# Kernel optimization log

Hardware: AMD Instinct MI355X
Metric: run time of the kernel (lower is better)

## Reference

```python
import jax, jax.numpy as jnp
import numpy as np

TAU = 2.0   # spikingjelly LIFNode default tau
VTH = 1.0   # config.vthreshold

@jax.custom_vjp
def atan_spike(x):
    # heaviside forward, ATan surrogate backward (spikingjelly surrogate.ATan, alpha=2)
    return (x >= 0).astype(x.dtype)

def _atan_fwd(x):
    return atan_spike(x), x

def _atan_bwd(x, g):
    alpha = 2.0
    return (g * (alpha / 2.0) / (1.0 + (jnp.pi / 2.0 * alpha * x) ** 2),)

atan_spike.defvjp(_atan_fwd, _atan_bwd)

def layer_norm(x, eps=1e-6):
    m = jnp.mean(x, axis=-1, keepdims=True)
    v = jnp.mean((x - m) ** 2, axis=-1, keepdims=True)
    return (x - m) * jax.lax.rsqrt(v + eps)

def time_shift(x):
    # ZeroPad2d((0,0,1,-1)): xx[:, t] = x[:, t-1], xx[:, 0] = 0
    return jnp.pad(x, ((0, 0), (1, 0), (0, 0)))[:, :-1]

def lif_multistep(x4):
    # spikingjelly LIFNode, step_mode='m', decay_input=True, hard reset to v_reset=0
    def step(v, xt):
        v = v + (xt - v) / TAU
        s = atan_spike(v - VTH)
        return v * (1.0 - s), s
    _, spikes = jax.lax.scan(step, jnp.zeros_like(x4[0]), x4)
    return spikes

def wkv(w, u, k, v):
    # RWKV-v4 numerically-stable WKV scan. w: [C] (negative), u: [C], k,v: [B,T,C]
    B, T, C = k.shape
    def step(carry, kv):
        aa, bb, pp = carry
        kt, vt = kv
        ww = u + kt
        p = jnp.maximum(pp, ww)
        e1 = jnp.exp(pp - p); e2 = jnp.exp(ww - p)
        y = (e1 * aa + e2 * vt) / (e1 * bb + e2)
        ww2 = pp + w
        p2 = jnp.maximum(ww2, kt)
        f1 = jnp.exp(ww2 - p2); f2 = jnp.exp(kt - p2)
        return (f1 * aa + f2 * vt, f1 * bb + f2, p2), y
    init = (jnp.zeros((B, C), k.dtype), jnp.zeros((B, C), k.dtype),
            jnp.full((B, C), -1e38, k.dtype))
    _, ys = jax.lax.scan(step, init, (jnp.moveaxis(k, 1, 0), jnp.moveaxis(v, 1, 0)))
    return jnp.moveaxis(ys, 0, 1)

def time_mix(h, time_decay, time_first, tmk, tmv, tmr, Wk, Wv, Wr, Wo):
    xx = time_shift(h)
    xk = h * tmk + xx * (1 - tmk)
    xv = h * tmv + xx * (1 - tmv)
    xr = h * tmr + xx * (1 - tmr)
    k = jnp.einsum('btc,oc->bto', xk, Wk)
    v = jnp.einsum('btc,oc->bto', xv, Wv)
    sr = jax.nn.sigmoid(jnp.einsum('btc,oc->bto', xr, Wr))
    y = wkv(-jnp.exp(time_decay), time_first, k, v)
    return jnp.einsum('btc,oc->bto', sr * y, Wo)

def channel_mix(h, cmk, cmr, Wck, Wcv, Wcr):
    xx = time_shift(h)
    xk = h * cmk + xx * (1 - cmk)
    xr = h * cmr + xx * (1 - cmr)
    k = jnp.square(jax.nn.relu(jnp.einsum('btc,hc->bth', xk, Wck)))
    kv = jnp.einsum('bth,ch->btc', k, Wcv)
    return jax.nn.sigmoid(jnp.einsum('btc,oc->bto', xr, Wcr)) * kv

def _forward(x, rt, time_decay, time_first, tmix_k, tmix_v, tmix_r,
             Wk, Wv, Wr, Wo, cmix_k, cmix_r, Wck, Wcv, Wcr,
             Wrm, brm, Wam, bam):
    B, P1, C = x.shape
    xc = jnp.concatenate([x, jnp.broadcast_to(rt, (B, P1, C))], axis=1)  # [B, 2*P1, C]
    att = time_mix(layer_norm(xc), time_decay, time_first,
                   tmix_k, tmix_v, tmix_r, Wk, Wv, Wr, Wo)
    att = lif_multistep(jnp.broadcast_to(att, (4,) + att.shape)).mean(0)
    xc = xc + att
    ffn = channel_mix(layer_norm(xc), cmix_k, cmix_r, Wck, Wcv, Wcr)
    ffn = lif_multistep(jnp.broadcast_to(ffn, (4,) + ffn.shape)).mean(0)
    xc = xc + ffn
    xo, rtok = xc[:, :P1], xc[:, P1:]
    r = jnp.einsum('bpc,qc->bpq', rtok, Wrm) + brm   # restruction_token_MLP [B,P1,P1]
    r = jnp.swapaxes(r, 1, 2)                        # permute(0,2,1)
    r = jnp.einsum('bpq,cq->bpc', r, Wam) + bam      # another_MLP [B,P1,C]
    return xo + xo * r

def setup_inputs() -> dict:
    key = jax.random.key(0)
    ks = jax.random.split(key, 20)
    B, P1, C = 8, 256, 1024
    H = 4 * C
    s = 0.02
    f32 = jnp.float32
    return {
        'x': jax.random.normal(ks[0], (B, P1, C), f32),
        'rt': jax.random.normal(ks[1], (1, P1, C), f32) * 0.5,
        'time_decay': jax.random.normal(ks[2], (C,), f32),
        'time_first': jax.random.normal(ks[3], (C,), f32) * 0.3,
        'tmix_k': jax.random.uniform(ks[4], (1, 1, C), f32),
        'tmix_v': jax.random.uniform(ks[5], (1, 1, C), f32),
        'tmix_r': jax.random.uniform(ks[6], (1, 1, C), f32),
        'Wk': jax.random.normal(ks[7], (C, C), f32) * s,
        'Wv': jax.random.normal(ks[8], (C, C), f32) * s,
        'Wr': jax.random.normal(ks[9], (C, C), f32) * s,
        'Wo': jax.random.normal(ks[10], (C, C), f32) * s,
        'cmix_k': jax.random.uniform(ks[11], (1, 1, C), f32),
        'cmix_r': jax.random.uniform(ks[12], (1, 1, C), f32),
        'Wck': jax.random.normal(ks[13], (H, C), f32) * s,
        'Wcv': jax.random.normal(ks[14], (C, H), f32) * s,
        'Wcr': jax.random.normal(ks[15], (C, C), f32) * s,
        'Wrm': jax.random.normal(ks[16], (P1, C), f32) * s,
        'brm': jax.random.normal(ks[17], (P1,), f32) * s,
        'Wam': jax.random.normal(ks[18], (C, P1), f32) * s,
        'bam': jax.random.normal(ks[19], (C,), f32) * s,
    }

def reference(x, rt, time_decay, time_first, tmix_k, tmix_v, tmix_r,
              Wk, Wv, Wr, Wo, cmix_k, cmix_r, Wck, Wcv, Wcr,
              Wrm, brm, Wam, bam):
    return _forward(x, rt, time_decay, time_first, tmix_k, tmix_v, tmix_r,
                    Wk, Wv, Wr, Wo, cmix_k, cmix_r, Wck, Wcv, Wcr,
                    Wrm, brm, Wam, bam)
```

## Files before the change

kernel.cpp:

```cpp
#include <hip/hip_runtime.h>
#include <hip/hip_bf16.h>
#include <math.h>
#include <stdint.h>

#define TB_ 8
#define TT_ 512
#define TC_ 1024
#define WKV_NCH 32
#define WKV_L 16

typedef __attribute__((ext_vector_type(8))) short bf16x8;
typedef __attribute__((ext_vector_type(4))) short s16x4;
typedef __attribute__((ext_vector_type(4))) float f32x4;

__device__ __forceinline__ float b2f(short u) {
  union { unsigned int i; float f; } x;
  x.i = ((unsigned int)(unsigned short)u) << 16;
  return x.f;
}
__device__ __forceinline__ short f2b(float f) {
  __hip_bfloat16 h = __float2bfloat16(f);
  return __builtin_bit_cast(short, h);
}
__device__ __forceinline__ float sigm(float x) { return 1.0f / (1.0f + expf(-x)); }

__device__ __forceinline__ float lif4(float a) {
  float v = 0.0f, acc = 0.0f;
#pragma unroll
  for (int i = 0; i < 4; ++i) {
    v += (a - v) * 0.5f;
    float s = (v >= 1.0f) ? 1.0f : 0.0f;
    acc += s;
    v *= (1.0f - s);
  }
  return acc * 0.25f;
}

__device__ __forceinline__ void gload16(const void* g, void* l) {
  __builtin_amdgcn_global_load_lds(
      (__attribute__((address_space(1))) void*)(g),
      (__attribute__((address_space(3))) void*)(l), 16, 0, 0);
}

template <int N>
__device__ __forceinline__ void waitv() {
  if constexpr (N == 0)  asm volatile("s_waitcnt vmcnt(0)" ::: "memory");
  else if constexpr (N == 2)  asm volatile("s_waitcnt vmcnt(2)" ::: "memory");
  else if constexpr (N == 4)  asm volatile("s_waitcnt vmcnt(4)" ::: "memory");
  else if constexpr (N == 8)  asm volatile("s_waitcnt vmcnt(8)" ::: "memory");
  else if constexpr (N == 12) asm volatile("s_waitcnt vmcnt(12)" ::: "memory");
  else static_assert(N == 0, "unsupported vmcnt");
}
__device__ __forceinline__ void barrier_() {
  asm volatile("s_barrier" ::: "memory");
}


__global__ __launch_bounds__(256) void ln_first(const float* __restrict__ x,
                                                const float* __restrict__ rt,
                                                float* __restrict__ xc,
                                                short* __restrict__ dst) {
  __shared__ float red[256];
  int row = blockIdx.x;
  int t = row & 511, b = row >> 9;
  const float* src = (t < 256) ? x + (int64_t)(b * 256 + t) * TC_
                               : rt + (int64_t)(t - 256) * TC_;
  float4 v = ((const float4*)src)[threadIdx.x];
  ((float4*)(xc + (int64_t)row * TC_))[threadIdx.x] = v;
  red[threadIdx.x] = v.x + v.y + v.z + v.w;
  __syncthreads();
  for (int off = 128; off > 0; off >>= 1) {
    if (threadIdx.x < off) red[threadIdx.x] += red[threadIdx.x + off];
    __syncthreads();
  }
  float mean = red[0] * (1.0f / 1024.0f);
  __syncthreads();
  float dx = v.x - mean, dy = v.y - mean, dz = v.z - mean, dw = v.w - mean;
  red[threadIdx.x] = dx * dx + dy * dy + dz * dz + dw * dw;
  __syncthreads();
  for (int off = 128; off > 0; off >>= 1) {
    if (threadIdx.x < off) red[threadIdx.x] += red[threadIdx.x + off];
    __syncthreads();
  }
  float rs = 1.0f / sqrtf(red[0] * (1.0f / 1024.0f) + 1e-6f);
  s16x4 o;
  o.x = f2b(dx * rs); o.y = f2b(dy * rs); o.z = f2b(dz * rs); o.w = f2b(dw * rs);
  *(s16x4*)(dst + (int64_t)row * TC_ + threadIdx.x * 4) = o;
}

__global__ __launch_bounds__(256) void ln_mix2(const float* __restrict__ xc,
                                               const float* __restrict__ cmk,
                                               const float* __restrict__ cmr,
                                               short* __restrict__ xk,
                                               short* __restrict__ xr) {
  __shared__ float red[256];
  int row = blockIdx.x;
  int t = row & 511;
  int tid = threadIdx.x;
  float4 v = ((const float4*)(xc + (int64_t)row * TC_))[tid];
  red[tid] = v.x + v.y + v.z + v.w;
  __syncthreads();
  for (int off = 128; off > 0; off >>= 1) {
    if (tid < off) red[tid] += red[tid + off];
    __syncthreads();
  }
  float mean = red[0] * (1.0f / 1024.0f);
  __syncthreads();
  float dx = v.x - mean, dy = v.y - mean, dz = v.z - mean, dw = v.w - mean;
  red[tid] = dx * dx + dy * dy + dz * dz + dw * dw;
  __syncthreads();
  for (int off = 128; off > 0; off >>= 1) {
    if (tid < off) red[tid] += red[tid + off];
    __syncthreads();
  }
  float rs = 1.0f / sqrtf(red[0] * (1.0f / 1024.0f) + 1e-6f);
  float c0 = dx * rs, c1 = dy * rs, c2 = dz * rs, c3 = dw * rs;
  float p0 = 0.f, p1 = 0.f, p2 = 0.f, p3 = 0.f;
  if (t > 0) {
    __syncthreads();
    float4 w4 = ((const float4*)(xc + (int64_t)(row - 1) * TC_))[tid];
    red[tid] = w4.x + w4.y + w4.z + w4.w;
    __syncthreads();
    for (int off = 128; off > 0; off >>= 1) {
      if (tid < off) red[tid] += red[tid + off];
      __syncthreads();
    }
    float meanp = red[0] * (1.0f / 1024.0f);
    __syncthreads();
    float ex = w4.x - meanp, ey = w4.y - meanp, ez = w4.z - meanp,
          ew = w4.w - meanp;
    red[tid] = ex * ex + ey * ey + ez * ez + ew * ew;
    __syncthreads();
    for (int off = 128; off > 0; off >>= 1) {
      if (tid < off) red[tid] += red[tid + off];
      __syncthreads();
    }
    float rsp = 1.0f / sqrtf(red[0] * (1.0f / 1024.0f) + 1e-6f);
    p0 = ex * rsp; p1 = ey * rsp; p2 = ez * rsp; p3 = ew * rsp;
  }
  int c = tid * 4;
  float k0 = cmk[c], k1 = cmk[c + 1], k2 = cmk[c + 2], k3 = cmk[c + 3];
  float r0 = cmr[c], r1 = cmr[c + 1], r2 = cmr[c + 2], r3 = cmr[c + 3];
  s16x4 ok, orr;
  ok.x = f2b(c0 * k0 + p0 * (1.0f - k0));
  ok.y = f2b(c1 * k1 + p1 * (1.0f - k1));
  ok.z = f2b(c2 * k2 + p2 * (1.0f - k2));
  ok.w = f2b(c3 * k3 + p3 * (1.0f - k3));
  orr.x = f2b(c0 * r0 + p0 * (1.0f - r0));
  orr.y = f2b(c1 * r1 + p1 * (1.0f - r1));
  orr.z = f2b(c2 * r2 + p2 * (1.0f - r2));
  orr.w = f2b(c3 * r3 + p3 * (1.0f - r3));
  *(s16x4*)(xk + (int64_t)row * TC_ + c) = ok;
  *(s16x4*)(xr + (int64_t)row * TC_ + c) = orr;
}

__global__ __launch_bounds__(256) void mix3_b(const short* __restrict__ ln,
                                              const float* __restrict__ tk,
                                              const float* __restrict__ tv,
                                              const float* __restrict__ tr,
                                              short* __restrict__ xk,
                                              short* __restrict__ xv,
                                              short* __restrict__ xr) {
  int i = blockIdx.x * 256 + threadIdx.x;
  int c8 = i & 127;
  int t = (i >> 7) & 511;
  bf16x8 h = *(const bf16x8*)(ln + (int64_t)i * 8);
  bf16x8 s = {};
  if (t > 0) s = *(const bf16x8*)(ln + (int64_t)(i - 128) * 8);
  bf16x8 ok, ov, orr;
#pragma unroll
  for (int e = 0; e < 8; ++e) {
    float hf = b2f(h[e]), sf = b2f(s[e]);
    int c = c8 * 8 + e;
    float mk = tk[c], mv = tv[c], mr = tr[c];
    ok[e] = f2b(hf * mk + sf * (1.0f - mk));
    ov[e] = f2b(hf * mv + sf * (1.0f - mv));
    orr[e] = f2b(hf * mr + sf * (1.0f - mr));
  }
  *(bf16x8*)(xk + (int64_t)i * 8) = ok;
  *(bf16x8*)(xv + (int64_t)i * 8) = ov;
  *(bf16x8*)(xr + (int64_t)i * 8) = orr;
}

__global__ __launch_bounds__(256) void cvt_b(const float* __restrict__ src,
                                             short* __restrict__ dst) {
  int64_t i = (int64_t)(blockIdx.x * 256 + threadIdx.x) * 8;
  float4 a = *(const float4*)(src + i);
  float4 b = *(const float4*)(src + i + 4);
  bf16x8 o;
  o[0] = f2b(a.x); o[1] = f2b(a.y); o[2] = f2b(a.z); o[3] = f2b(a.w);
  o[4] = f2b(b.x); o[5] = f2b(b.y); o[6] = f2b(b.z); o[7] = f2b(b.w);
  *(bf16x8*)(dst + i) = o;
}

__global__ __launch_bounds__(256) void cvt_all(
    const float* __restrict__ Wk, const float* __restrict__ Wv,
    const float* __restrict__ Wr, const float* __restrict__ Wo,
    const float* __restrict__ Wcr, const float* __restrict__ Wcv,
    const float* __restrict__ Wrm, const float* __restrict__ Wam,
    short* __restrict__ bWk, short* __restrict__ bWv, short* __restrict__ bWr,
    short* __restrict__ bWo, short* __restrict__ bWcr, short* __restrict__ bWcv,
    short* __restrict__ bWrm, short* __restrict__ bWam,
    float* __restrict__ S) {
  int bid = blockIdx.x;
  if (bid >= 4864) {
    int row = (bid - 4864) * 4 + (threadIdx.x >> 6);
    int lane = threadIdx.x & 63;
    float4 v = ((const float4*)(Wam + (int64_t)row * 256))[lane];
    float s = v.x + v.y + v.z + v.w;
    for (int off = 32; off > 0; off >>= 1) s += __shfl_down(s, off);
    if (lane == 0) S[row] = s;
    return;
  }
  const float* src; short* dst; int base;
  if (bid < 512)       { src = Wk;  dst = bWk;  base = bid; }
  else if (bid < 1024) { src = Wv;  dst = bWv;  base = bid - 512; }
  else if (bid < 1536) { src = Wr;  dst = bWr;  base = bid - 1024; }
  else if (bid < 2048) { src = Wo;  dst = bWo;  base = bid - 1536; }
  else if (bid < 2560) { src = Wcr; dst = bWcr; base = bid - 2048; }
  else if (bid < 4608) { src = Wcv; dst = bWcv; base = bid - 2560; }
  else if (bid < 4736) { src = Wrm; dst = bWrm; base = bid - 4608; }
  else                 { src = Wam; dst = bWam; base = bid - 4736; }
  int64_t i = ((int64_t)base * 256 + threadIdx.x) * 8;
  float4 a = *(const float4*)(src + i);
  float4 b = *(const float4*)(src + i + 4);
  bf16x8 o;
  o[0] = f2b(a.x); o[1] = f2b(a.y); o[2] = f2b(a.z); o[3] = f2b(a.w);
  o[4] = f2b(b.x); o[5] = f2b(b.y); o[6] = f2b(b.z); o[7] = f2b(b.w);
  *(bf16x8*)(dst + i) = o;
}

__global__ __launch_bounds__(256) void wkv_p1(const float* __restrict__ td,
                                              const short* __restrict__ K,
                                              const short* __restrict__ V,
                                              float* __restrict__ Ca,
                                              float* __restrict__ Da,
                                              float* __restrict__ Qa) {
  int bx = blockIdx.x;
  int ch = bx >> 5;
  int b = (bx >> 2) & 7;
  int c = (bx & 3) * 256 + threadIdx.x;
  float w = -expf(td[c]);
  float aa = 0.0f, bb = 0.0f, pp = -1e38f;
  int64_t base = ((int64_t)b * TT_ + ch * WKV_L) * TC_ + c;
#pragma unroll
  for (int t = 0; t < WKV_L; ++t) {
    int64_t o = base + (int64_t)t * TC_;
    float kt = b2f(K[o]), vt = b2f(V[o]);
    float ww2 = pp + w;
    float p2 = fmaxf(ww2, kt);
    float e1 = expf(ww2 - p2);
    float e2 = expf(kt - p2);
    aa = e1 * aa + e2 * vt;
    bb = e1 * bb + e2;
    pp = p2;
  }
  int idx = ch * 8192 + b * 1024 + c;
  Ca[idx] = aa; Da[idx] = bb; Qa[idx] = pp;
}

__global__ __launch_bounds__(256) void wkv_p2(const float* __restrict__ td,
                                              const float* __restrict__ Ca,
                                              const float* __restrict__ Da,
                                              const float* __restrict__ Qa,
                                              float* __restrict__ Aa,
                                              float* __restrict__ Ba,
                                              float* __restrict__ Pa) {
  int i = blockIdx.x * 256 + threadIdx.x;
  int c = i & (TC_ - 1);
  float wL = -expf(td[c]) * (float)WKV_L;
  float aa = 0.0f, bb = 0.0f, pp = -1e38f;
#pragma unroll 4
  for (int ch = 0; ch < WKV_NCH; ++ch) {
    int idx = ch * 8192 + i;
    Aa[idx] = aa; Ba[idx] = bb; Pa[idx] = pp;
    float ppw = pp + wL;
    float q = Qa[idx];
    float p2 = fmaxf(ppw, q);
    float ea = expf(ppw - p2);
    float eb = expf(q - p2);
    aa = aa * ea + Ca[idx] * eb;
    bb = bb * ea + Da[idx] * eb;
    pp = p2;
  }
}

__global__ __launch_bounds__(256) void wkv_p3(const float* __restrict__ td,
                                              const float* __restrict__ tf,
                                              const short* __restrict__ K,
                                              const short* __restrict__ V,
                                              const short* __restrict__ SR,
                                              short* __restrict__ SRY,
                                              const float* __restrict__ Aa,
                                              const float* __restrict__ Ba,
                                              const float* __restrict__ Pa) {
  int bx = blockIdx.x;
  int ch = bx >> 5;
  int b = (bx >> 2) & 7;
  int c = (bx & 3) * 256 + threadIdx.x;
  float w = -expf(td[c]);
  float u = tf[c];
  int idx = ch * 8192 + b * 1024 + c;
  float aa = Aa[idx], bb = Ba[idx], pp = Pa[idx];
  int64_t base = ((int64_t)b * TT_ + ch * WKV_L) * TC_ + c;
#pragma unroll
  for (int t = 0; t < WKV_L; ++t) {
    int64_t o = base + (int64_t)t * TC_;
    float kt = b2f(K[o]), vt = b2f(V[o]);
    float ww = u + kt;
    float p = fmaxf(pp, ww);
    float E1 = expf(pp - p);
    float E2 = expf(ww - p);
    float y = (E1 * aa + E2 * vt) / (E1 * bb + E2);
    SRY[o] = f2b(y * b2f(SR[o]));
    float ww2 = pp + w;
    float p2 = fmaxf(ww2, kt);
    float e1 = expf(ww2 - p2);
    float e2 = expf(kt - p2);
    aa = e1 * aa + e2 * vt;
    bb = e1 * bb + e2;
    pp = p2;
  }
}

template <int BM, int BN, int EPI, int D, int MINW>
__global__ __launch_bounds__(256, MINW) void gemm_bf16(
    const short* __restrict__ A, const short* __restrict__ B,
    void* __restrict__ Cp, int M, int N, int K, int Kst,
    int64_t sA, int64_t sB, int64_t sC,
    const float* __restrict__ e0, const float* __restrict__ e1,
    const float* __restrict__ e2, const void* __restrict__ e3, int64_t sE) {
  constexpr int MF = BM / 32;
  constexpr int NF = BN / 32;
  constexpr int ASLOT = BM / 64;
  constexpr int BSLOT = BN / 64;
  constexpr int NL = ASLOT + BSLOT;
  constexpr int SBUF = (BM + BN) * 32;
  __shared__ short lds[D * SBUF];
  const int tid = threadIdx.x;

  const unsigned gx = gridDim.x, gy = gridDim.y;
  const unsigned nwg = gx * gy * gridDim.z;
  const unsigned lin = blockIdx.x + gx * (blockIdx.y + gy * blockIdx.z);
  const unsigned cs = nwg >> 3;
  const unsigned nl = (lin & 7) * cs + (lin >> 3);
  const unsigned bxs = nl % gx;
  const unsigned tmp = nl / gx;
  const unsigned bys = tmp % gy;
  const unsigned bz = tmp / gy;

  const int brow = bys * BM;
  const int bcol = bxs * BN;
  const short* Ab = A + bz * sA;
  const short* Bb = B + bz * sB;

  const int srow = ((tid >> 6) << 4) + (tid & 15);
  const int skc = ((tid >> 4) & 3) * 8;
  const short* gA[ASLOT];
  const short* gB[BSLOT];
#pragma unroll
  for (int s = 0; s < ASLOT; ++s)
    gA[s] = Ab + (int64_t)(brow + s * 64 + srow) * Kst + skc;
#pragma unroll
  for (int s = 0; s < BSLOT; ++s)
    gB[s] = Bb + (int64_t)(bcol + s * 64 + srow) * Kst + skc;

  const int lane = tid & 63, wid = tid >> 6;
  const int wr = wid >> 1, wc = wid & 1;

  f32x4 acc[MF][NF] = {};

  auto stage = [&](int buf, int k0) {
    short* d = lds + buf * SBUF;
#pragma unroll
    for (int s = 0; s < ASLOT; ++s)
      gload16(gA[s] + k0, d + s * 2048 + tid * 8);
#pragma unroll
    for (int s = 0; s < BSLOT; ++s)
      gload16(gB[s] + k0, d + BM * 32 + s * 2048 + tid * 8);
  };
  auto compute = [&](int buf) {
    const short* base = lds + buf * SBUF;
    bf16x8 af[MF], bfv[NF];
#pragma unroll
    for (int m = 0; m < MF; ++m)
      af[m] = *(const bf16x8*)(base + (wr * MF + m) * 512 + lane * 8);
#pragma unroll
    for (int n = 0; n < NF; ++n)
      bfv[n] = *(const bf16x8*)(base + BM * 32 + (wc * NF + n) * 512 + lane * 8);
#pragma unroll
    for (int m = 0; m < MF; ++m)
#pragma unroll
      for (int n = 0; n < NF; ++n)
        acc[m][n] = __builtin_amdgcn_mfma_f32_16x16x32_bf16(af[m], bfv[n],
                                                            acc[m][n], 0, 0, 0);
  };

  const int nst = K / 32;
#pragma unroll
  for (int d = 0; d < D - 1; ++d) stage(d, d * 32);
  for (int t = 0; t <= nst - D; ++t) {
    stage((t + D - 1) & (D - 1), (t + D - 1) * 32);
    waitv<(D - 1) * NL>();
    barrier_();
    compute(t & (D - 1));
    barrier_();
  }
  {
    int t = nst - D + 1;
    if constexpr (D >= 4) {
      waitv<2 * NL>(); barrier_(); compute(t & (D - 1)); barrier_(); ++t;
      waitv<1 * NL>(); barrier_(); compute(t & (D - 1)); barrier_(); ++t;
    }
    waitv<0>(); barrier_(); compute(t & (D - 1));
  }

  const int r0 = brow + wr * (BM / 2) + (lane >> 4) * 4;
  const int c0 = bcol + wc * (BN / 2) + (lane & 15);
#pragma unroll
  for (int m = 0; m < MF; ++m) {
#pragma unroll
    for (int j = 0; j < 4; ++j) {
      int row = r0 + m * 16 + j;
#pragma unroll
      for (int n = 0; n < NF; ++n) {
        int col = c0 + n * 16;
        float v = acc[m][n][j];
        int64_t idx = (int64_t)row * N + col;
        if (EPI == 0) {
          ((short*)Cp)[bz * sC + idx] = f2b(v);
        } else if (EPI == 1) {
          ((short*)Cp)[bz * sC + idx] = f2b(sigm(v));
        } else if (EPI == 2) {
          v = fmaxf(v, 0.0f);
          ((short*)Cp)[bz * sC + idx] = f2b(v * v);
        } else if (EPI == 3) {
          float r2 = v + e0[row] * e1[col] + e2[col];
          float xo = ((const float*)e3)[bz * sE + idx];
          ((float*)Cp)[bz * sC + idx] = xo * (1.0f + r2);
        } else if (EPI == 4) {
          float* XC = (float*)Cp;
          XC[idx] = XC[idx] + lif4(v);
        } else if (EPI == 5) {
          float* XC = (float*)Cp;
          float srr = b2f(((const short*)e3)[idx]);
          float nv = XC[idx] + lif4(v * srr);
          XC[idx] = nv;
          int tt = row & 511;
          if (tt >= 256) {
            short* rtok = (short*)(void*)const_cast<float*>(e1);
            rtok[(((int64_t)(row >> 9)) * 256 + (tt - 256)) * 1024 + col] =
                f2b(nv);
          }
        } else if (EPI == 6) {
          ((short*)Cp)[bz * sC + idx] = f2b(bz == 2 ? sigm(v) : v);
        }
      }
    }
  }
}

extern "C" void kernel_launch(void* const* d_in, const int* in_sizes, int n_in,
                              void* d_out, int out_size, void* d_ws,
                              size_t ws_size, hipStream_t stream) {
  const float* x   = (const float*)d_in[0];
  const float* rt  = (const float*)d_in[1];
  const float* td  = (const float*)d_in[2];
  const float* tf  = (const float*)d_in[3];
  const float* tmk = (const float*)d_in[4];
  const float* tmv = (const float*)d_in[5];
  const float* tmr = (const float*)d_in[6];
  const float* Wk  = (const float*)d_in[7];
  const float* Wv  = (const float*)d_in[8];
  const float* Wr  = (const float*)d_in[9];
  const float* Wo  = (const float*)d_in[10];
  const float* cmk = (const float*)d_in[11];
  const float* cmr = (const float*)d_in[12];
  const float* Wck = (const float*)d_in[13];
  const float* Wcv = (const float*)d_in[14];
  const float* Wcr = (const float*)d_in[15];
  const float* Wrm = (const float*)d_in[16];
  const float* brm = (const float*)d_in[17];
  const float* Wam = (const float*)d_in[18];
  const float* bam = (const float*)d_in[19];
  float* out = (float*)d_out;

  const size_t MB = 1ull << 20;
  uint8_t* W8 = (uint8_t*)d_ws;
  float* XC   = (float*)(W8);
  short* L    = (short*)(W8 + 16 * MB);
  short* S1   = (short*)(W8 + 24 * MB);
  short* S2   = (short*)(W8 + 32 * MB);
  short* S3   = (short*)(W8 + 40 * MB);
  short* bWcv = (short*)(W8 + 48 * MB);
  short* bWk  = (short*)(W8 + 56 * MB);
  short* bWo  = (short*)(W8 + 62 * MB);
  short* bWcr = (short*)(W8 + 64 * MB);
  short* bWrm = (short*)(W8 + 66 * MB);
  short* bWam = (short*)(W8 + 66 * MB + 512 * 1024);
  short* KK   = (short*)(W8 + 67 * MB);
  short* VV   = (short*)(W8 + 75 * MB);
  short* RR   = (short*)(W8 + 83 * MB);
  float* Ca   = (float*)(W8 + 91 * MB);
  float* Da   = (float*)(W8 + 92 * MB);
  float* Qa   = (float*)(W8 + 93 * MB);
  float* Aa   = (float*)(W8 + 94 * MB);
  float* Ba   = (float*)(W8 + 95 * MB);
  float* Pa   = (float*)(W8 + 96 * MB);
  short* SRY  = S1;
  short* xk2  = S2;
  short* xr2  = S3;
  short* SRR  = S1;
  short* bWck = S3;
  short* H16  = KK;
  short* rtok = S2;
  short* Mt   = (short*)(W8 + 36 * MB);
  float* Sb   = (float*)(W8 + 99 * MB);

  dim3 blk(256);
  const int NV8 = 2048;

  cvt_all<<<5120, blk, 0, stream>>>(Wk, Wv, Wr, Wo, Wcr, Wcv, Wrm, Wam,
                                    bWk, bWk + 1048576, bWk + 2097152, bWo,
                                    bWcr, bWcv, bWrm, bWam, Sb);

  ln_first<<<TB_ * TT_, blk, 0, stream>>>(x, rt, XC, L);
  mix3_b<<<NV8, blk, 0, stream>>>(L, tmk, tmv, tmr, S1, S2, S3);

  gemm_bf16<128, 128, 6, 2, 3><<<dim3(8, 32, 3), blk, 0, stream>>>(
      S1, bWk, KK, 4096, 1024, 1024, 1024, 4194304, 1048576, 4194304,
      nullptr, nullptr, nullptr, nullptr, 0);
  wkv_p1<<<WKV_NCH * TB_ * 4, blk, 0, stream>>>(td, KK, VV, Ca, Da, Qa);
  wkv_p2<<<32, blk, 0, stream>>>(td, Ca, Da, Qa, Aa, Ba, Pa);
  wkv_p3<<<WKV_NCH * TB_ * 4, blk, 0, stream>>>(td, tf, KK, VV, RR, SRY,
                                                Aa, Ba, Pa);
  gemm_bf16<128, 128, 4, 4, 2><<<dim3(8, 32, 1), blk, 0, stream>>>(
      SRY, bWo, XC, 4096, 1024, 1024, 1024, 0, 0, 0,
      nullptr, nullptr, nullptr, nullptr, 0);
  ln_mix2<<<TB_ * TT_, blk, 0, stream>>>(XC, cmk, cmr, xk2, xr2);
  gemm_bf16<128, 128, 1, 4, 2><<<dim3(8, 32, 1), blk, 0, stream>>>(
      xr2, bWcr, SRR, 4096, 1024, 1024, 1024, 0, 0, 0,
      nullptr, nullptr, nullptr, nullptr, 0);
  cvt_b<<<2048, blk, 0, stream>>>(Wck, bWck);
  gemm_bf16<128, 128, 2, 2, 4><<<dim3(32, 32, 1), blk, 0, stream>>>(
      xk2, bWck, H16, 4096, 4096, 1024, 1024, 0, 0, 0,
      nullptr, nullptr, nullptr, nullptr, 0);
  gemm_bf16<128, 128, 5, 4, 2><<<dim3(8, 32, 1), blk, 0, stream>>>(
      H16, bWcv, XC, 4096, 1024, 4096, 4096, 0, 0, 0,
      nullptr, (const float*)rtok, nullptr, SRR, 0);
  gemm_bf16<64, 64, 0, 2, 2><<<dim3(4, 4, 8), blk, 0, stream>>>(
      bWrm, rtok, Mt, 256, 256, 1024, 1024, 0, (int64_t)256 * 1024,
      (int64_t)256 * 256, nullptr, nullptr, nullptr, nullptr, 0);
  gemm_bf16<64, 64, 3, 2, 2><<<dim3(16, 4, 8), blk, 0, stream>>>(
      Mt, bWam, out, 256, 1024, 256, 256, (int64_t)256 * 256, 0,
      (int64_t)256 * 1024, brm, Sb, bam, XC, (int64_t)512 * 1024);
}
```

Measured before the change: 343.4 us.

## Split GEMM K dimension across two warp groups with LDS reduction

Adds a GROUPS template parameter so a 512-thread block runs two 256-thread groups, each computing half of the K range with its own LDS buffers. The groups then sum their partial accumulators through shared memory before the epilogue. Four of the 128x128 GEMMs (Wo, Wcr, Wck, Wcv) switch to this intra-block split-K with pipeline depth 2. The aim is more waves in flight per tile to hide latency on the low-tile-count GEMMs, at the cost of an extra LDS reduction and changed occupancy and pipeline depth.

```diff
diff --git a/kernel.cpp b/kernel.cpp
--- a/kernel.cpp
+++ b/kernel.cpp
@@ -323,8 +323,8 @@
   }
 }
 
-template <int BM, int BN, int EPI, int D, int MINW>
-__global__ __launch_bounds__(256, MINW) void gemm_bf16(
+template <int BM, int BN, int EPI, int D, int MINW, int GROUPS>
+__global__ __launch_bounds__(256 * GROUPS, MINW) void gemm_bf16(
     const short* __restrict__ A, const short* __restrict__ B,
     void* __restrict__ Cp, int M, int N, int K, int Kst,
     int64_t sA, int64_t sB, int64_t sC,
@@ -336,8 +336,11 @@
   constexpr int BSLOT = BN / 64;
   constexpr int NL = ASLOT + BSLOT;
   constexpr int SBUF = (BM + BN) * 32;
-  __shared__ short lds[D * SBUF];
+  __shared__ short lds[GROUPS * D * SBUF];
   const int tid = threadIdx.x;
+  const int gtid = tid & 255;
+  const int grp = (GROUPS > 1) ? (tid >> 8) : 0;
+  short* glds = lds + grp * D * SBUF;
 
   const unsigned gx = gridDim.x, gy = gridDim.y;
   const unsigned nwg = gx * gy * gridDim.z;
@@ -351,11 +354,13 @@
 
   const int brow = bys * BM;
   const int bcol = bxs * BN;
-  const short* Ab = A + bz * sA;
-  const short* Bb = B + bz * sB;
-
-  const int srow = ((tid >> 6) << 4) + (tid & 15);
-  const int skc = ((tid >> 4) & 3) * 8;
+  const int kbeg = grp * (K / GROUPS);
+  const int ksteps = (K / GROUPS) / 32;
+  const short* Ab = A + bz * sA + kbeg;
+  const short* Bb = B + bz * sB + kbeg;
+
+  const int srow = ((gtid >> 6) << 4) + (gtid & 15);
+  const int skc = ((gtid >> 4) & 3) * 8;
   const short* gA[ASLOT];
   const short* gB[BSLOT];
 #pragma unroll
@@ -365,22 +370,22 @@
   for (int s = 0; s < BSLOT; ++s)
     gB[s] = Bb + (int64_t)(bcol + s * 64 + srow) * Kst + skc;
 
-  const int lane = tid & 63, wid = tid >> 6;
+  const int lane = gtid & 63, wid = gtid >> 6;
   const int wr = wid >> 1, wc = wid & 1;
 
   f32x4 acc[MF][NF] = {};
 
   auto stage = [&](int buf, int k0) {
-    short* d = lds + buf * SBUF;
+    short* d = glds + buf * SBUF;
 #pragma unroll
     for (int s = 0; s < ASLOT; ++s)
-      gload16(gA[s] + k0, d + s * 2048 + tid * 8);
+      gload16(gA[s] + k0, d + s * 2048 + gtid * 8);
 #pragma unroll
     for (int s = 0; s < BSLOT; ++s)
-      gload16(gB[s] + k0, d + BM * 32 + s * 2048 + tid * 8);
+      gload16(gB[s] + k0, d + BM * 32 + s * 2048 + gtid * 8);
   };
   auto compute = [&](int buf) {
-    const short* base = lds + buf * SBUF;
+    const short* base = glds + buf * SBUF;
     bf16x8 af[MF], bfv[NF];
 #pragma unroll
     for (int m = 0; m < MF; ++m)
@@ -396,10 +401,9 @@
                                                             acc[m][n], 0, 0, 0);
   };
 
-  const int nst = K / 32;
 #pragma unroll
   for (int d = 0; d < D - 1; ++d) stage(d, d * 32);
-  for (int t = 0; t <= nst - D; ++t) {
+  for (int t = 0; t <= ksteps - D; ++t) {
     stage((t + D - 1) & (D - 1), (t + D - 1) * 32);
     waitv<(D - 1) * NL>();
     barrier_();
@@ -407,12 +411,35 @@
     barrier_();
   }
   {
-    int t = nst - D + 1;
+    int t = ksteps - D + 1;
     if constexpr (D >= 4) {
       waitv<2 * NL>(); barrier_(); compute(t & (D - 1)); barrier_(); ++t;
       waitv<1 * NL>(); barrier_(); compute(t & (D - 1)); barrier_(); ++t;
     }
     waitv<0>(); barrier_(); compute(t & (D - 1));
+  }
+
+  if constexpr (GROUPS == 2) {
+    __syncthreads();
+    float* red = (float*)lds;
+    if (grp == 1) {
+#pragma unroll
+      for (int m = 0; m < MF; ++m)
+#pragma unroll
+        for (int n = 0; n < NF; ++n)
+#pragma unroll
+          for (int j = 0; j < 4; ++j)
+            red[(((m * NF) + n) * 4 + j) * 256 + gtid] = acc[m][n][j];
+    }
+    __syncthreads();
+    if (grp != 0) return;
+#pragma unroll
+    for (int m = 0; m < MF; ++m)
+#pragma unroll
+      for (int n = 0; n < NF; ++n)
+#pragma unroll
+        for (int j = 0; j < 4; ++j)
+          acc[m][n][j] += red[(((m * NF) + n) * 4 + j) * 256 + gtid];
   }
 
   const int r0 = brow + wr * (BM / 2) + (lane >> 4) * 4;
@@ -518,6 +545,7 @@
   float* Sb   = (float*)(W8 + 99 * MB);
 
   dim3 blk(256);
+  dim3 blk2(512);
   const int NV8 = 2048;
 
   cvt_all<<<5120, blk, 0, stream>>>(Wk, Wv, Wr, Wo, Wcr, Wcv, Wrm, Wam,
@@ -527,31 +555,31 @@
   ln_first<<<TB_ * TT_, blk, 0, stream>>>(x, rt, XC, L);
   mix3_b<<<NV8, blk, 0, stream>>>(L, tmk, tmv, tmr, S1, S2, S3);
 
-  gemm_bf16<128, 128, 6, 2, 3><<<dim3(8, 32, 3), blk, 0, stream>>>(
+  gemm_bf16<128, 128, 6, 2, 3, 1><<<dim3(8, 32, 3), blk, 0, stream>>>(
       S1, bWk, KK, 4096, 1024, 1024, 1024, 4194304, 1048576, 4194304,
       nullptr, nullptr, nullptr, nullptr, 0);
   wkv_p1<<<WKV_NCH * TB_ * 4, blk, 0, stream>>>(td, KK, VV, Ca, Da, Qa);
   wkv_p2<<<32, blk, 0, stream>>>(td, Ca, Da, Qa, Aa, Ba, Pa);
   wkv_p3<<<WKV_NCH * TB_ * 4, blk, 0, stream>>>(td, tf, KK, VV, RR, SRY,
                                                 Aa, Ba, Pa);
-  gemm_bf16<128, 128, 4, 4, 2><<<dim3(8, 32, 1), blk, 0, stream>>>(
+  gemm_bf16<128, 128, 4, 2, 1, 2><<<dim3(8, 32, 1), blk2, 0, stream>>>(
       SRY, bWo, XC, 4096, 1024, 1024, 1024, 0, 0, 0,
       nullptr, nullptr, nullptr, nullptr, 0);
   ln_mix2<<<TB_ * TT_, blk, 0, stream>>>(XC, cmk, cmr, xk2, xr2);
-  gemm_bf16<128, 128, 1, 4, 2><<<dim3(8, 32, 1), blk, 0, stream>>>(
+  gemm_bf16<128, 128, 1, 2, 1, 2><<<dim3(8, 32, 1), blk2, 0, stream>>>(
       xr2, bWcr, SRR, 4096, 1024, 1024, 1024, 0, 0, 0,
       nullptr, nullptr, nullptr, nullptr, 0);
   cvt_b<<<2048, blk, 0, stream>>>(Wck, bWck);
-  gemm_bf16<128, 128, 2, 2, 4><<<dim3(32, 32, 1), blk, 0, stream>>>(
+  gemm_bf16<128, 128, 2, 2, 1, 2><<<dim3(32, 32, 1), blk2, 0, stream>>>(
       xk2, bWck, H16, 4096, 4096, 1024, 1024, 0, 0, 0,
       nullptr, nullptr, nullptr, nullptr, 0);
-  gemm_bf16<128, 128, 5, 4, 2><<<dim3(8, 32, 1), blk, 0, stream>>>(
+  gemm_bf16<128, 128, 5, 2, 1, 2><<<dim3(8, 32, 1), blk2, 0, stream>>>(
       H16, bWcv, XC, 4096, 1024, 4096, 4096, 0, 0, 0,
       nullptr, (const float*)rtok, nullptr, SRR, 0);
-  gemm_bf16<64, 64, 0, 2, 2><<<dim3(4, 4, 8), blk, 0, stream>>>(
+  gemm_bf16<64, 64, 0, 2, 2, 1><<<dim3(4, 4, 8), blk, 0, stream>>>(
       bWrm, rtok, Mt, 256, 256, 1024, 1024, 0, (int64_t)256 * 1024,
       (int64_t)256 * 256, nullptr, nullptr, nullptr, nullptr, 0);
-  gemm_bf16<64, 64, 3, 2, 2><<<dim3(16, 4, 8), blk, 0, stream>>>(
+  gemm_bf16<64, 64, 3, 2, 2, 1><<<dim3(16, 4, 8), blk, 0, stream>>>(
       Mt, bWam, out, 256, 1024, 256, 256, (int64_t)256 * 256, 0,
       (int64_t)256 * 1024, brm, Sb, bam, XC, (int64_t)512 * 1024);
 }
```

Result: no change. 348.0 us (+1.3%).
